# Kernel tuning notes

Hardware: AMD Instinct MI355X
Metric: run time of the kernel (lower is better)

## Reference

```python
import jax, jax.numpy as jnp
import numpy as np

NUM_CLASSES = 10
F_THRESH = 0.0
O_THRESH = 0.0


def setup_inputs() -> dict:
    key = jax.random.key(0)
    k1, k2, k3 = jax.random.split(key, 3)
    B, TS, C, H, W = 64, 128, 1, 64, 64
    x = jax.random.normal(k1, (B, TS, C, H, W), dtype=jnp.float32)
    # nn.Linear(64*64, num_classes): weight [num_classes, 4096], bias [num_classes]
    fan_in = C * H * W
    bound = 1.0 / np.sqrt(fan_in)
    Wfc = jax.random.uniform(k2, (NUM_CLASSES, fan_in), minval=-bound, maxval=bound, dtype=jnp.float32)
    bfc = jax.random.uniform(k3, (NUM_CLASSES,), minval=-bound, maxval=bound, dtype=jnp.float32)
    return {"input": x, "Wfc": Wfc, "bfc": bfc}


def reference(input, Wfc, bfc):
    # input: [B, TS, C, H, W]
    B, TS, C, H, W = input.shape
    h0 = input[:, 0]                                   # [B, C, H, W]
    frames = jnp.moveaxis(input[:, 1:], 1, 0)          # [TS-1, B, C, H, W]
    acc0 = jnp.zeros((B, NUM_CLASSES), dtype=input.dtype)

    def step(carry, frame):
        h_next, acc = carry
        diff = frame - h_next
        forget_gate = jnp.where(diff * diff > F_THRESH * F_THRESH, 1.0, 0.0)
        out_gate = jnp.where(diff * diff <= O_THRESH * O_THRESH, 0.0, 1.0)
        sign = jnp.where(diff > O_THRESH, 1.0, -1.0)
        out_next = out_gate * sign                      # [B, C, H, W]
        h_new = forget_gate * diff + h_next
        logits = out_next.reshape(B, -1) @ Wfc.T + bfc  # [B, num_classes]
        return (h_new, acc + logits), None

    (_, out), _ = jax.lax.scan(step, (h0, acc0), frames)
    return out / TS
```

## Files before the change

kernel.cpp:

```cpp
#include <hip/hip_runtime.h>

#ifndef NUM_CLASSES
#define NUM_CLASSES 10
#endif

constexpr int B_        = 64;
constexpr int TS_       = 128;
constexpr int K_        = 4096;
constexpr int THREADS_  = 512;
constexpr int TCHUNKS_  = 8;
constexpr int TSTEP_    = 16;
constexpr int NPART_    = TCHUNKS_;
constexpr int NWAVES_   = THREADS_ / 64;

__global__ __launch_bounds__(THREADS_) void sign_fc_kernel(
    const float* __restrict__ x, const float* __restrict__ Wfc,
    float* __restrict__ P)
{
    const int b   = blockIdx.x;
    const int tc  = blockIdx.y;
    const int tid = threadIdx.x;

    const int t_begin = tc * TSTEP_;
    const int t_end   = (tc == TCHUNKS_ - 1) ? (TS_ - 1) : (t_begin + TSTEP_);

    const int kbase = tid * 4;

    const float* xp = x + ((size_t)b * TS_ + t_begin) * K_ + kbase;
    float4 prev0 = *reinterpret_cast<const float4*>(xp);
    float4 prev1 = *reinterpret_cast<const float4*>(xp + 2048);

    int s0 = 0, s1 = 0, s2 = 0, s3 = 0, s4 = 0, s5 = 0, s6 = 0, s7 = 0;

#pragma unroll 4
    for (int t = t_begin + 1; t <= t_end; ++t) {
        xp += K_;
        const float4 cur0 = *reinterpret_cast<const float4*>(xp);
        const float4 cur1 = *reinterpret_cast<const float4*>(xp + 2048);
        float d;
        d = cur0.x - prev0.x; s0 += (d > 0.0f) - (d < 0.0f);
        d = cur0.y - prev0.y; s1 += (d > 0.0f) - (d < 0.0f);
        d = cur0.z - prev0.z; s2 += (d > 0.0f) - (d < 0.0f);
        d = cur0.w - prev0.w; s3 += (d > 0.0f) - (d < 0.0f);
        d = cur1.x - prev1.x; s4 += (d > 0.0f) - (d < 0.0f);
        d = cur1.y - prev1.y; s5 += (d > 0.0f) - (d < 0.0f);
        d = cur1.z - prev1.z; s6 += (d > 0.0f) - (d < 0.0f);
        d = cur1.w - prev1.w; s7 += (d > 0.0f) - (d < 0.0f);
        prev0 = cur0;
        prev1 = cur1;
    }

    const float f0 = (float)s0, f1 = (float)s1, f2 = (float)s2, f3 = (float)s3;
    const float f4 = (float)s4, f5 = (float)s5, f6 = (float)s6, f7 = (float)s7;

    float acc[NUM_CLASSES];
#pragma unroll
    for (int c = 0; c < NUM_CLASSES; ++c) {
        const float* wr = Wfc + (size_t)c * K_ + kbase;
        const float4 w0 = *reinterpret_cast<const float4*>(wr);
        const float4 w1 = *reinterpret_cast<const float4*>(wr + 2048);
        acc[c] = f0 * w0.x + f1 * w0.y + f2 * w0.z + f3 * w0.w
               + f4 * w1.x + f5 * w1.y + f6 * w1.z + f7 * w1.w;
    }

#pragma unroll
    for (int off = 32; off > 0; off >>= 1) {
#pragma unroll
        for (int c = 0; c < NUM_CLASSES; ++c)
            acc[c] += __shfl_down(acc[c], off, 64);
    }

    __shared__ float red[NUM_CLASSES][NWAVES_];
    const int wave = tid >> 6;
    const int lane = tid & 63;
    if (lane == 0) {
#pragma unroll
        for (int c = 0; c < NUM_CLASSES; ++c) red[c][wave] = acc[c];
    }
    __syncthreads();

    if (tid < NUM_CLASSES) {
        float v = 0.0f;
#pragma unroll
        for (int w = 0; w < NWAVES_; ++w) v += red[tid][w];
        P[((size_t)b * NUM_CLASSES + tid) * NPART_ + tc] = v;
    }
}

__global__ __launch_bounds__(64) void fc_finish_kernel(
    const float* __restrict__ P, const float* __restrict__ bfc,
    float* __restrict__ out)
{
    const int b = blockIdx.x;
    const int c = threadIdx.x;
    if (c >= NUM_CLASSES) return;

    const float* p = P + ((size_t)b * NUM_CLASSES + c) * NPART_;
    float s = 0.0f;
#pragma unroll
    for (int i = 0; i < NPART_; ++i) s += p[i];

    out[b * NUM_CLASSES + c] = (s + (float)(TS_ - 1) * bfc[c]) * (1.0f / (float)TS_);
}

extern "C" void kernel_launch(void* const* d_in, const int* in_sizes, int n_in,
                              void* d_out, int out_size, void* d_ws, size_t ws_size,
                              hipStream_t stream)
{
    const float* x   = (const float*)d_in[0];
    const float* Wfc = (const float*)d_in[1];
    const float* bfc = (const float*)d_in[2];
    float* out = (float*)d_out;
    float* P = (float*)d_ws;

    dim3 grid1(B_, TCHUNKS_);
    sign_fc_kernel<<<grid1, THREADS_, 0, stream>>>(x, Wfc, P);

    fc_finish_kernel<<<B_, 64, 0, stream>>>(P, bfc, out);
}
```

Before: 29.99 us.

## Fuse finish reduction into main kernel via last-block atomic ticket, use nontemporal loads

Result: slower. 46.93 us (+56.5%).

```diff
diff --git a/kernel.cpp b/kernel.cpp
--- a/kernel.cpp
+++ b/kernel.cpp
@@ -12,14 +12,26 @@
 constexpr int TSTEP_    = 16;
 constexpr int NPART_    = TCHUNKS_;
 constexpr int NWAVES_   = THREADS_ / 64;
+constexpr int NBLOCKS_  = B_ * TCHUNKS_;
+constexpr int NTICKETS_ = NBLOCKS_ * NUM_CLASSES;
 
-__global__ __launch_bounds__(THREADS_) void sign_fc_kernel(
+typedef float f32x4 __attribute__((ext_vector_type(4)));
+
+__device__ __forceinline__ f32x4 nt_load4(const float* p) {
+    return __builtin_nontemporal_load(reinterpret_cast<const f32x4*>(p));
+}
+
+__global__ __launch_bounds__(THREADS_) void sign_fc_fused_kernel(
     const float* __restrict__ x, const float* __restrict__ Wfc,
-    float* __restrict__ P)
+    const float* __restrict__ bfc, float* __restrict__ out,
+    float* __restrict__ P, unsigned int* __restrict__ cnt)
 {
     const int b   = blockIdx.x;
     const int tc  = blockIdx.y;
     const int tid = threadIdx.x;
+
+    __shared__ int sh_last;
+    if (tid == 0) sh_last = 0;
 
     const int t_begin = tc * TSTEP_;
     const int t_end   = (tc == TCHUNKS_ - 1) ? (TS_ - 1) : (t_begin + TSTEP_);
@@ -27,16 +39,16 @@
     const int kbase = tid * 4;
 
     const float* xp = x + ((size_t)b * TS_ + t_begin) * K_ + kbase;
-    float4 prev0 = *reinterpret_cast<const float4*>(xp);
-    float4 prev1 = *reinterpret_cast<const float4*>(xp + 2048);
+    f32x4 prev0 = nt_load4(xp);
+    f32x4 prev1 = nt_load4(xp + 2048);
 
     int s0 = 0, s1 = 0, s2 = 0, s3 = 0, s4 = 0, s5 = 0, s6 = 0, s7 = 0;
 
 #pragma unroll 4
     for (int t = t_begin + 1; t <= t_end; ++t) {
         xp += K_;
-        const float4 cur0 = *reinterpret_cast<const float4*>(xp);
-        const float4 cur1 = *reinterpret_cast<const float4*>(xp + 2048);
+        const f32x4 cur0 = nt_load4(xp);
+        const f32x4 cur1 = nt_load4(xp + 2048);
         float d;
         d = cur0.x - prev0.x; s0 += (d > 0.0f) - (d < 0.0f);
         d = cur0.y - prev0.y; s1 += (d > 0.0f) - (d < 0.0f);
@@ -84,23 +96,23 @@
 #pragma unroll
         for (int w = 0; w < NWAVES_; ++w) v += red[tid][w];
         P[((size_t)b * NUM_CLASSES + tid) * NPART_ + tc] = v;
+        __threadfence();
+        const unsigned old = atomicAdd(cnt, 1u);
+        if (old == (unsigned)(NTICKETS_ - 1)) sh_last = 1;
     }
-}
+    __syncthreads();
 
-__global__ __launch_bounds__(64) void fc_finish_kernel(
-    const float* __restrict__ P, const float* __restrict__ bfc,
-    float* __restrict__ out)
-{
-    const int b = blockIdx.x;
-    const int c = threadIdx.x;
-    if (c >= NUM_CLASSES) return;
-
-    const float* p = P + ((size_t)b * NUM_CLASSES + c) * NPART_;
-    float s = 0.0f;
+    if (sh_last) {
+        __threadfence();
+        for (int idx = tid; idx < B_ * NUM_CLASSES; idx += THREADS_) {
+            const int c = idx % NUM_CLASSES;
+            const float* p = P + (size_t)idx * NPART_;
+            float s = 0.0f;
 #pragma unroll
-    for (int i = 0; i < NPART_; ++i) s += p[i];
-
-    out[b * NUM_CLASSES + c] = (s + (float)(TS_ - 1) * bfc[c]) * (1.0f / (float)TS_);
+            for (int i = 0; i < NPART_; ++i) s += p[i];
+            out[idx] = (s + (float)(TS_ - 1) * bfc[c]) * (1.0f / (float)TS_);
+        }
+    }
 }
 
 extern "C" void kernel_launch(void* const* d_in, const int* in_sizes, int n_in,
@@ -111,10 +123,12 @@
     const float* Wfc = (const float*)d_in[1];
     const float* bfc = (const float*)d_in[2];
     float* out = (float*)d_out;
+
     float* P = (float*)d_ws;
+    unsigned int* cnt = (unsigned int*)((char*)d_ws + B_ * NUM_CLASSES * NPART_ * sizeof(float));
 
-    dim3 grid1(B_, TCHUNKS_);
-    sign_fc_kernel<<<grid1, THREADS_, 0, stream>>>(x, Wfc, P);
+    (void)hipMemsetAsync(cnt, 0, sizeof(unsigned int), stream);
 
-    fc_finish_kernel<<<B_, 64, 0, stream>>>(P, bfc, out);
+    dim3 grid(B_, TCHUNKS_);
+    sign_fc_fused_kernel<<<grid, THREADS_, 0, stream>>>(x, Wfc, bfc, out, P, cnt);
 }
```
